# Performance work log

Hardware: AMD Instinct MI355X
Metric: run time of the kernel (lower is better)

## Reference

```python
import jax, jax.numpy as jnp
import numpy as np

N = 200000
K = 16
D = 32
IN_SIZE = K * (K - 1) // 2  # 120
HID = 128


def setup_inputs() -> dict:
    key = jax.random.key(0)
    ks = jax.random.split(key, 12)
    E = N * K
    x = jax.random.normal(ks[0], (N, D), dtype=jnp.float32)
    edge_attr = jax.random.normal(ks[1], (E, D), dtype=jnp.float32)
    # kNN-style edge_index: source node i owns edges [i*K, (i+1)*K)
    src = jnp.repeat(jnp.arange(N, dtype=jnp.int64), K)
    dst = jax.random.randint(ks[2], (E,), 0, N, dtype=jnp.int64)
    edge_index = jnp.stack([src, dst], axis=0)
    s = 0.1
    W1 = jax.random.normal(ks[3], (IN_SIZE, HID), dtype=jnp.float32) * s
    b1 = jnp.zeros((HID,), dtype=jnp.float32)
    W2 = jax.random.normal(ks[4], (HID, HID), dtype=jnp.float32) * s
    b2 = jnp.zeros((HID,), dtype=jnp.float32)
    W3 = jax.random.normal(ks[5], (HID, HID), dtype=jnp.float32) * s
    b3 = jnp.zeros((HID,), dtype=jnp.float32)
    W4 = jax.random.normal(ks[6], (HID, 1), dtype=jnp.float32) * s
    b4 = jnp.zeros((1,), dtype=jnp.float32)
    return {"x": x, "edge_index": edge_index, "edge_attr": edge_attr, "k": K,
            "W1": W1, "b1": b1, "W2": W2, "b2": b2, "W3": W3, "b3": b3,
            "W4": W4, "b4": b4}


def calc_pair_angles(edge_attr, k):
    # edge_attr: [N*k, d] per-edge neighbor vectors, grouped k per node
    E, d = edge_attr.shape
    n = E // k
    v = edge_attr.reshape(n, k, d)
    vn = v / (jnp.linalg.norm(v, axis=-1, keepdims=True) + 1e-12)
    cos = jnp.einsum('nkd,nmd->nkm', vn, vn)  # [n, k, k]
    cos = jnp.clip(cos, -1.0 + 1e-7, 1.0 - 1e-7)
    ang = jnp.arccos(cos)
    iu, ju = jnp.triu_indices(k, 1)
    return ang[:, iu, ju]  # [n, k*(k-1)/2]


def reference(x, edge_index, edge_attr, k, W1, b1, W2, b2, W3, b3, W4, b4):
    # message() returns edge_attr; aggregate() computes pairwise neighbor angles
    feats = calc_pair_angles(edge_attr, k)  # [N, 120]
    h = jnp.tanh(feats @ W1 + b1)
    h = jnp.tanh(h @ W2 + b2)
    h = jnp.tanh(h @ W3 + b3)
    out = jax.nn.sigmoid(h @ W4 + b4)  # [N, 1]
    return out[:, 0]  # squeeze, [N]
```

## Files before the change

kernel.cpp:

```cpp
#include <hip/hip_runtime.h>
#include <hip/hip_bf16.h>
#include <math.h>


#define CHUNK     32
#define NTHREADS  256
#define ASTRIDE   136

typedef _Float16 f16;
typedef f16  f16x8 __attribute__((ext_vector_type(8)));
typedef f16  f16x4 __attribute__((ext_vector_type(4)));
typedef float f32x4 __attribute__((ext_vector_type(4)));

__device__ __forceinline__ float fast_tanh(float x) {
    float e = __expf(2.0f * x);
    return 1.0f - 2.0f * __builtin_amdgcn_rcpf(e + 1.0f);
}

__device__ __forceinline__ float fast_acos(float x) {
    float ax = fabsf(x);
    float p = fmaf(-0.0187293f, ax, 0.0742610f);
    p = fmaf(p, ax, -0.2121144f);
    p = fmaf(p, ax, 1.5707288f);
    float r = sqrtf(1.0f - ax) * p;
    return (x >= 0.0f) ? r : (3.14159265358979f - r);
}

__global__ void prep_weights(const float* __restrict__ W1,
                             const float* __restrict__ W2,
                             const float* __restrict__ W3,
                             f16* __restrict__ wt)
{
    int tid = blockIdx.x * 256 + threadIdx.x;
    if (tid >= 3 * 128 * 128) return;
    int layer = tid >> 14;
    int rem   = tid & 16383;
    int j     = rem >> 7;
    int i     = rem & 127;
    const float* W = (layer == 0) ? W1 : ((layer == 1) ? W2 : W3);
    int in_l = (layer == 0) ? 120 : 128;
    float v = (i < in_l) ? W[i * 128 + j] : 0.0f;
    wt[tid] = (f16)v;
}

__device__ __forceinline__ void gram_acos_node(float4 c0, float4 c1, int m,
                                               int lr, int lg, f16* actA)
{
    float ss = c0.x*c0.x + c0.y*c0.y + c0.z*c0.z + c0.w*c0.w
             + c1.x*c1.x + c1.y*c1.y + c1.z*c1.z + c1.w*c1.w;
    ss += __shfl_xor(ss, 16);
    ss += __shfl_xor(ss, 32);
    const float sc = __builtin_amdgcn_rsqf(ss + 1e-24f);
    f16x8 frag;
    frag[0] = (f16)(c0.x * sc); frag[1] = (f16)(c0.y * sc);
    frag[2] = (f16)(c0.z * sc); frag[3] = (f16)(c0.w * sc);
    frag[4] = (f16)(c1.x * sc); frag[5] = (f16)(c1.y * sc);
    frag[6] = (f16)(c1.z * sc); frag[7] = (f16)(c1.w * sc);
    f32x4 acc = {0.f, 0.f, 0.f, 0.f};
    acc = __builtin_amdgcn_mfma_f32_16x16x32_f16(frag, frag, acc, 0, 0, 0);
    const int col = lr;
    #pragma unroll
    for (int r2 = 0; r2 < 4; ++r2) {
        const int row = lg * 4 + r2;
        float c = fminf(fmaxf(acc[r2], -1.0f + 1e-7f), 1.0f - 1e-7f);
        float ang = fast_acos(c);
        if (row < col) {
            const int p = 15 * row - ((row * (row - 1)) >> 1) + (col - row - 1);
            actA[m * ASTRIDE + p] = (f16)ang;
        }
    }
}

__device__ __forceinline__ void mlp_layer_mfma(const f16* __restrict__ wl,
                                               const float* __restrict__ bias,
                                               const f16* src, f16* dst,
                                               int w, int lr, int lg)
{
    #pragma unroll
    for (int jj = 0; jj < 2; ++jj) {
        const int jt = w * 2 + jj;
        const f16* wr = wl + (jt * 16 + lr) * 128 + lg * 8;
        f16x8 a0 = *(const f16x8*)(wr);
        f16x8 a1 = *(const f16x8*)(wr + 32);
        f16x8 a2 = *(const f16x8*)(wr + 64);
        f16x8 a3 = *(const f16x8*)(wr + 96);
        f32x4 bv = *(const f32x4*)(bias + jt * 16 + lg * 4);
        #pragma unroll
        for (int nt = 0; nt < 2; ++nt) {
            const int node = nt * 16 + lr;
            const f16* sr = src + node * ASTRIDE + lg * 8;
            f16x8 bf0 = *(const f16x8*)(sr);
            f16x8 bf1 = *(const f16x8*)(sr + 32);
            f16x8 bf2 = *(const f16x8*)(sr + 64);
            f16x8 bf3 = *(const f16x8*)(sr + 96);
            f32x4 acc = {0.f, 0.f, 0.f, 0.f};
            acc = __builtin_amdgcn_mfma_f32_16x16x32_f16(a0, bf0, acc, 0, 0, 0);
            acc = __builtin_amdgcn_mfma_f32_16x16x32_f16(a1, bf1, acc, 0, 0, 0);
            acc = __builtin_amdgcn_mfma_f32_16x16x32_f16(a2, bf2, acc, 0, 0, 0);
            acc = __builtin_amdgcn_mfma_f32_16x16x32_f16(a3, bf3, acc, 0, 0, 0);
            f16x4 o;
            #pragma unroll
            for (int r = 0; r < 4; ++r)
                o[r] = (f16)fast_tanh(acc[r] + bv[r]);
            *(f16x4*)(dst + node * ASTRIDE + jt * 16 + lg * 4) = o;
        }
    }
}

__global__ __launch_bounds__(NTHREADS, 3)
void gnn_angle_fused(const float* __restrict__ edge_attr,
                     const f16*   __restrict__ wt,
                     const float* __restrict__ b1, const float* __restrict__ b2,
                     const float* __restrict__ b3,
                     const float* __restrict__ W4, const float* __restrict__ b4,
                     float* __restrict__ out, int n_nodes)
{
    __shared__ __attribute__((aligned(16))) f16 actA[CHUNK * ASTRIDE];
    __shared__ __attribute__((aligned(16))) f16 actB[CHUNK * ASTRIDE];

    const int t = threadIdx.x;
    const int w = t >> 6;
    const int l = t & 63;
    const int base = blockIdx.x * CHUNK;
    const int lr = l & 15;
    const int lg = l >> 4;

    actA[(t >> 3) * ASTRIDE + 120 + (t & 7)] = (f16)0.f;

    const float* sw = edge_attr + ((long)base + w) * 512 + lr * 32 + lg * 8;

    if (base + CHUNK <= n_nodes) {
        float4 d0a = *(const float4*)(sw +     0), d0b = *(const float4*)(sw +     4);
        float4 d1a = *(const float4*)(sw +  2048), d1b = *(const float4*)(sw +  2052);
        float4 d2a = *(const float4*)(sw +  4096), d2b = *(const float4*)(sw +  4100);
        float4 d3a = *(const float4*)(sw +  6144), d3b = *(const float4*)(sw +  6148);
        float4 d4a = *(const float4*)(sw +  8192), d4b = *(const float4*)(sw +  8196);
        float4 d5a = *(const float4*)(sw + 10240), d5b = *(const float4*)(sw + 10244);
        float4 d6a = *(const float4*)(sw + 12288), d6b = *(const float4*)(sw + 12292);
        float4 d7a = *(const float4*)(sw + 14336), d7b = *(const float4*)(sw + 14340);
        gram_acos_node(d0a, d0b, w +  0, lr, lg, actA);
        gram_acos_node(d1a, d1b, w +  4, lr, lg, actA);
        gram_acos_node(d2a, d2b, w +  8, lr, lg, actA);
        gram_acos_node(d3a, d3b, w + 12, lr, lg, actA);
        gram_acos_node(d4a, d4b, w + 16, lr, lg, actA);
        gram_acos_node(d5a, d5b, w + 20, lr, lg, actA);
        gram_acos_node(d6a, d6b, w + 24, lr, lg, actA);
        gram_acos_node(d7a, d7b, w + 28, lr, lg, actA);
    } else {
        for (int c = 0; c < 8; ++c) {
            const int m = c * 4 + w;
            const long g = (long)base + m;
            if (g < n_nodes) {
                const float* s = sw + (long)c * 2048;
                float4 c0 = *(const float4*)(s);
                float4 c1 = *(const float4*)(s + 4);
                gram_acos_node(c0, c1, m, lr, lg, actA);
            }
        }
    }
    __syncthreads();

    mlp_layer_mfma(wt,             b1, actA, actB, w, lr, lg);
    __syncthreads();
    mlp_layer_mfma(wt + 16384,     b2, actB, actA, w, lr, lg);
    __syncthreads();
    mlp_layer_mfma(wt + 2 * 16384, b3, actA, actB, w, lr, lg);
    __syncthreads();

    {
        const int node = t >> 3;
        const int part = t & 7;
        const int i0 = part * 16;
        const f16* sr = actB + node * ASTRIDE + i0;
        f16x8 h0 = *(const f16x8*)(sr);
        f16x8 h1 = *(const f16x8*)(sr + 8);
        float s = 0.f;
        #pragma unroll
        for (int e = 0; e < 8; ++e) s = fmaf((float)h0[e], W4[i0 + e], s);
        #pragma unroll
        for (int e = 0; e < 8; ++e) s = fmaf((float)h1[e], W4[i0 + 8 + e], s);
        s += __shfl_xor(s, 1);
        s += __shfl_xor(s, 2);
        s += __shfl_xor(s, 4);
        if (part == 0) {
            const long g = (long)base + node;
            if (g < n_nodes)
                out[g] = __builtin_amdgcn_rcpf(1.0f + __expf(-(s + b4[0])));
        }
    }
}

extern "C" void kernel_launch(void* const* d_in, const int* in_sizes, int n_in,
                              void* d_out, int out_size, void* d_ws, size_t ws_size,
                              hipStream_t stream) {
    const float* edge_attr = (const float*)d_in[2];
    const float* W1 = (const float*)d_in[4];
    const float* b1 = (const float*)d_in[5];
    const float* W2 = (const float*)d_in[6];
    const float* b2 = (const float*)d_in[7];
    const float* W3 = (const float*)d_in[8];
    const float* b3 = (const float*)d_in[9];
    const float* W4 = (const float*)d_in[10];
    const float* b4 = (const float*)d_in[11];
    float* out = (float*)d_out;
    f16* wt = (f16*)d_ws;

    const int n_nodes = in_sizes[2] / 512;

    prep_weights<<<(3 * 128 * 128 + 255) / 256, 256, 0, stream>>>(W1, W2, W3, wt);

    const int blocks = (n_nodes + CHUNK - 1) / CHUNK;
    gnn_angle_fused<<<blocks, NTHREADS, 0, stream>>>(
        edge_attr, wt, b1, b2, b3, W4, b4, out, n_nodes);
}
```

Baseline: 138.9 us.

## Make fused GNN kernel persistent with register prefetch of next chunk

Replaces the one-block-per-chunk grid with a persistent grid of 768 blocks that loop over node chunks. Inside the loop, each block loads the edge_attr data for its next chunk into registers while the MLP layers run on the current chunk, so global-memory latency overlaps with MFMA work. The prefetch doubles the live float4 registers, which may reduce occupancy under the 3-blocks-per-SM launch bound. A fixed 768-block grid may also not match the CU count well.

Result: slower. 223.3 us (+60.8%).

```diff
diff --git a/kernel.cpp b/kernel.cpp
--- a/kernel.cpp
+++ b/kernel.cpp
@@ -3,9 +3,10 @@
 #include <math.h>
 
 
-#define CHUNK     32
-#define NTHREADS  256
-#define ASTRIDE   136
+#define NTHREADS 256
+#define CHUNK    32
+#define ASTRIDE  136
+#define PBLOCKS  768
 
 typedef _Float16 f16;
 typedef f16  f16x8 __attribute__((ext_vector_type(8)));
@@ -44,7 +45,7 @@
 }
 
 __device__ __forceinline__ void gram_acos_node(float4 c0, float4 c1, int m,
-                                               int lr, int lg, f16* actA)
+                                               int lr, int lg, f16* actF)
 {
     float ss = c0.x*c0.x + c0.y*c0.y + c0.z*c0.z + c0.w*c0.w
              + c1.x*c1.x + c1.y*c1.y + c1.z*c1.z + c1.w*c1.w;
@@ -66,7 +67,7 @@
         float ang = fast_acos(c);
         if (row < col) {
             const int p = 15 * row - ((row * (row - 1)) >> 1) + (col - row - 1);
-            actA[m * ASTRIDE + p] = (f16)ang;
+            actF[m * ASTRIDE + p] = (f16)ang;
         }
     }
 }
@@ -108,12 +109,12 @@
 }
 
 __global__ __launch_bounds__(NTHREADS, 3)
-void gnn_angle_fused(const float* __restrict__ edge_attr,
-                     const f16*   __restrict__ wt,
-                     const float* __restrict__ b1, const float* __restrict__ b2,
-                     const float* __restrict__ b3,
-                     const float* __restrict__ W4, const float* __restrict__ b4,
-                     float* __restrict__ out, int n_nodes)
+void gnn_persist(const float* __restrict__ edge_attr,
+                 const f16*   __restrict__ wt,
+                 const float* __restrict__ b1, const float* __restrict__ b2,
+                 const float* __restrict__ b3,
+                 const float* __restrict__ W4, const float* __restrict__ b4,
+                 float* __restrict__ out, int n_nodes, int nchunks)
 {
     __shared__ __attribute__((aligned(16))) f16 actA[CHUNK * ASTRIDE];
     __shared__ __attribute__((aligned(16))) f16 actB[CHUNK * ASTRIDE];
@@ -121,23 +122,30 @@
     const int t = threadIdx.x;
     const int w = t >> 6;
     const int l = t & 63;
-    const int base = blockIdx.x * CHUNK;
     const int lr = l & 15;
     const int lg = l >> 4;
 
     actA[(t >> 3) * ASTRIDE + 120 + (t & 7)] = (f16)0.f;
 
-    const float* sw = edge_attr + ((long)base + w) * 512 + lr * 32 + lg * 8;
-
-    if (base + CHUNK <= n_nodes) {
-        float4 d0a = *(const float4*)(sw +     0), d0b = *(const float4*)(sw +     4);
-        float4 d1a = *(const float4*)(sw +  2048), d1b = *(const float4*)(sw +  2052);
-        float4 d2a = *(const float4*)(sw +  4096), d2b = *(const float4*)(sw +  4100);
-        float4 d3a = *(const float4*)(sw +  6144), d3b = *(const float4*)(sw +  6148);
-        float4 d4a = *(const float4*)(sw +  8192), d4b = *(const float4*)(sw +  8196);
-        float4 d5a = *(const float4*)(sw + 10240), d5b = *(const float4*)(sw + 10244);
-        float4 d6a = *(const float4*)(sw + 12288), d6b = *(const float4*)(sw + 12292);
-        float4 d7a = *(const float4*)(sw + 14336), d7b = *(const float4*)(sw + 14340);
+    #define LOADN(da, db, c, ch)                                                \
+        {                                                                       \
+            const long gn = (long)(ch) * CHUNK + (c) * 4 + w;                   \
+            da = make_float4(0.f,0.f,0.f,0.f); db = da;                         \
+            if (gn < n_nodes) {                                                 \
+                const float* s = edge_attr + gn * 512 + lr * 32 + lg * 8;       \
+                da = *(const float4*)(s);                                       \
+                db = *(const float4*)(s + 4);                                   \
+            }                                                                   \
+        }
+
+    long chunk = blockIdx.x;
+    float4 d0a,d0b,d1a,d1b,d2a,d2b,d3a,d3b,d4a,d4b,d5a,d5b,d6a,d6b,d7a,d7b;
+    LOADN(d0a,d0b,0,chunk) LOADN(d1a,d1b,1,chunk)
+    LOADN(d2a,d2b,2,chunk) LOADN(d3a,d3b,3,chunk)
+    LOADN(d4a,d4b,4,chunk) LOADN(d5a,d5b,5,chunk)
+    LOADN(d6a,d6b,6,chunk) LOADN(d7a,d7b,7,chunk)
+
+    for (; chunk < nchunks; chunk += PBLOCKS) {
         gram_acos_node(d0a, d0b, w +  0, lr, lg, actA);
         gram_acos_node(d1a, d1b, w +  4, lr, lg, actA);
         gram_acos_node(d2a, d2b, w +  8, lr, lg, actA);
@@ -146,48 +154,52 @@
         gram_acos_node(d5a, d5b, w + 20, lr, lg, actA);
         gram_acos_node(d6a, d6b, w + 24, lr, lg, actA);
         gram_acos_node(d7a, d7b, w + 28, lr, lg, actA);
-    } else {
-        for (int c = 0; c < 8; ++c) {
-            const int m = c * 4 + w;
-            const long g = (long)base + m;
-            if (g < n_nodes) {
-                const float* s = sw + (long)c * 2048;
-                float4 c0 = *(const float4*)(s);
-                float4 c1 = *(const float4*)(s + 4);
-                gram_acos_node(c0, c1, m, lr, lg, actA);
+
+        const long nxt = chunk + PBLOCKS;
+        float4 e0a,e0b,e1a,e1b,e2a,e2b,e3a,e3b,e4a,e4b,e5a,e5b,e6a,e6b,e7a,e7b;
+        e0a=e0b=e1a=e1b=e2a=e2b=e3a=e3b=make_float4(0.f,0.f,0.f,0.f);
+        e4a=e4b=e5a=e5b=e6a=e6b=e7a=e7b=e0a;
+        if (nxt < nchunks) {
+            LOADN(e0a,e0b,0,nxt) LOADN(e1a,e1b,1,nxt)
+            LOADN(e2a,e2b,2,nxt) LOADN(e3a,e3b,3,nxt)
+            LOADN(e4a,e4b,4,nxt) LOADN(e5a,e5b,5,nxt)
+            LOADN(e6a,e6b,6,nxt) LOADN(e7a,e7b,7,nxt)
+        }
+        __syncthreads();
+
+        mlp_layer_mfma(wt,             b1, actA, actB, w, lr, lg);
+        __syncthreads();
+        mlp_layer_mfma(wt + 16384,     b2, actB, actA, w, lr, lg);
+        __syncthreads();
+        mlp_layer_mfma(wt + 2 * 16384, b3, actA, actB, w, lr, lg);
+        __syncthreads();
+
+        {
+            const int node = t >> 3;
+            const int part = t & 7;
+            const int i0 = part * 16;
+            const f16* sr = actB + node * ASTRIDE + i0;
+            f16x8 h0 = *(const f16x8*)(sr);
+            f16x8 h1 = *(const f16x8*)(sr + 8);
+            float s = 0.f;
+            #pragma unroll
+            for (int e = 0; e < 8; ++e) s = fmaf((float)h0[e], W4[i0 + e], s);
+            #pragma unroll
+            for (int e = 0; e < 8; ++e) s = fmaf((float)h1[e], W4[i0 + 8 + e], s);
+            s += __shfl_xor(s, 1);
+            s += __shfl_xor(s, 2);
+            s += __shfl_xor(s, 4);
+            if (part == 0) {
+                const long g = chunk * CHUNK + node;
+                if (g < n_nodes)
+                    out[g] = __builtin_amdgcn_rcpf(1.0f + __expf(-(s + b4[0])));
             }
         }
+
+        d0a=e0a; d0b=e0b; d1a=e1a; d1b=e1b; d2a=e2a; d2b=e2b; d3a=e3a; d3b=e3b;
+        d4a=e4a; d4b=e4b; d5a=e5a; d5b=e5b; d6a=e6a; d6b=e6b; d7a=e7a; d7b=e7b;
     }
-    __syncthreads();
-
-    mlp_layer_mfma(wt,             b1, actA, actB, w, lr, lg);
-    __syncthreads();
-    mlp_layer_mfma(wt + 16384,     b2, actB, actA, w, lr, lg);
-    __syncthreads();
-    mlp_layer_mfma(wt + 2 * 16384, b3, actA, actB, w, lr, lg);
-    __syncthreads();
-
-    {
-        const int node = t >> 3;
-        const int part = t & 7;
-        const int i0 = part * 16;
-        const f16* sr = actB + node * ASTRIDE + i0;
-        f16x8 h0 = *(const f16x8*)(sr);
-        f16x8 h1 = *(const f16x8*)(sr + 8);
-        float s = 0.f;
-        #pragma unroll
-        for (int e = 0; e < 8; ++e) s = fmaf((float)h0[e], W4[i0 + e], s);
-        #pragma unroll
-        for (int e = 0; e < 8; ++e) s = fmaf((float)h1[e], W4[i0 + 8 + e], s);
-        s += __shfl_xor(s, 1);
-        s += __shfl_xor(s, 2);
-        s += __shfl_xor(s, 4);
-        if (part == 0) {
-            const long g = (long)base + node;
-            if (g < n_nodes)
-                out[g] = __builtin_amdgcn_rcpf(1.0f + __expf(-(s + b4[0])));
-        }
-    }
+    #undef LOADN
 }
 
 extern "C" void kernel_launch(void* const* d_in, const int* in_sizes, int n_in,
@@ -206,10 +218,11 @@
     f16* wt = (f16*)d_ws;
 
     const int n_nodes = in_sizes[2] / 512;
+    const int nchunks = (n_nodes + CHUNK - 1) / CHUNK;
+    const int blocks  = PBLOCKS < nchunks ? PBLOCKS : nchunks;
 
     prep_weights<<<(3 * 128 * 128 + 255) / 256, 256, 0, stream>>>(W1, W2, W3, wt);
 
-    const int blocks = (n_nodes + CHUNK - 1) / CHUNK;
-    gnn_angle_fused<<<blocks, NTHREADS, 0, stream>>>(
-        edge_attr, wt, b1, b2, b3, W4, b4, out, n_nodes);
-}
+    gnn_persist<<<blocks, NTHREADS, 0, stream>>>(
+        edge_attr, wt, b1, b2, b3, W4, b4, out, n_nodes, nchunks);
+}
```
